# Optimization experiments

Hardware: AMD Instinct MI355X
Metric: run time of the kernel (lower is better)

## Reference

```python
import jax, jax.numpy as jnp
import numpy as np

NUM_EMBED = 1024
NUM_HEADS = 16
BLOCK_SIZE = 2048


def setup_inputs() -> dict:
    key = jax.random.key(0)
    k1, k2, k3, k4, k5 = jax.random.split(key, 5)
    C = NUM_EMBED
    s = 1.0 / np.sqrt(C)
    x = jax.random.normal(k1, (2, BLOCK_SIZE, C), dtype=jnp.float32)
    # nn.Linear params: weight (out,in), bias (out,)
    w_attn = jax.random.uniform(k2, (3 * C, C), minval=-s, maxval=s, dtype=jnp.float32)
    b_attn = jax.random.uniform(k3, (3 * C,), minval=-s, maxval=s, dtype=jnp.float32)
    w_proj = jax.random.uniform(k4, (C, C), minval=-s, maxval=s, dtype=jnp.float32)
    b_proj = jax.random.uniform(k5, (C,), minval=-s, maxval=s, dtype=jnp.float32)
    return {"x": x, "w_attn": w_attn, "b_attn": b_attn, "w_proj": w_proj, "b_proj": b_proj}


def reference(x, w_attn, b_attn, w_proj, b_proj):
    B, T, C = x.shape
    H = NUM_HEADS
    D = C // H
    kqv = jnp.einsum('btc,oc->bto', x, w_attn) + b_attn  # (B,T,3C)
    # Original code splits as K, Q, V in that order.
    K, Q, V = jnp.split(kqv, 3, axis=2)
    K = K.reshape(B, T, H, D).transpose(0, 2, 1, 3)  # (B,H,T,D)
    Q = Q.reshape(B, T, H, D).transpose(0, 2, 1, 3)
    V = V.reshape(B, T, H, D).transpose(0, 2, 1, 3)
    aff = jnp.einsum('bhqd,bhkd->bhqk', Q, K) * (D ** -0.5)  # (B,H,T,T)
    causal = jnp.tril(jnp.ones((T, T), dtype=bool))
    aff = jnp.where(causal[None, None], aff, jnp.float32(-jnp.inf))
    wei = jax.nn.softmax(aff, axis=-1)
    attn = jnp.einsum('bhqk,bhkd->bhqd', wei, V)
    attn = attn.transpose(0, 2, 1, 3).reshape(B, T, C)
    out = jnp.einsum('btc,oc->bto', attn, w_proj) + b_proj
    return out
```

## Files before the change

kernel.cpp:

```cpp
#include <hip/hip_runtime.h>
#include <cstdint>

typedef __attribute__((ext_vector_type(8))) short bf16x8;
typedef __attribute__((ext_vector_type(4))) float f32x4;
typedef __attribute__((ext_vector_type(4))) uint16_t u16x4;

__device__ __forceinline__ uint16_t f2b(float f) {
  union { float f; uint32_t i; } v; v.f = f;
  return (uint16_t)((v.i + 0x7FFFu + ((v.i >> 16) & 1u)) >> 16);
}

#define GLDS16(g, l) __builtin_amdgcn_global_load_lds( \
    (const __attribute__((address_space(1))) void*)(g), \
    (__attribute__((address_space(3))) void*)(l), 16, 0, 0)

__global__ __launch_bounds__(256) void cvt_f32_bf16(
    const float* __restrict__ src, uint16_t* __restrict__ dst, int n) {
  const int i = (blockIdx.x * 256 + threadIdx.x) * 4;
  if (i + 3 < n) {
    const float4 v = *(const float4*)(src + i);
    u16x4 o;
    o.x = f2b(v.x); o.y = f2b(v.y); o.z = f2b(v.z); o.w = f2b(v.w);
    *(u16x4*)(dst + i) = o;
  }
}

template <int BM, bool OUT_BF16>
__global__ __launch_bounds__(256) void gemm_bt_bias(
    const uint16_t* __restrict__ A, const uint16_t* __restrict__ B,
    const float* __restrict__ bias, void* __restrict__ Cv,
    int M, int N, int K) {
  constexpr int MI = BM / 32;
  constexpr int CA = BM / 16;
  constexpr int CPW = (2 * (CA + 8)) / 4;
  constexpr int CT_PITCH = OUT_BF16 ? 72 : 68;
  constexpr size_t CT_BYTES = (size_t)4 * (BM / 2) * CT_PITCH * (OUT_BF16 ? 2 : 4);
  constexpr size_t ST_BYTES = (size_t)(2 * (BM * 32 + 4096)) * 2;
  constexpr size_t LB = CT_BYTES > ST_BYTES ? CT_BYTES : ST_BYTES;
  __shared__ alignas(16) unsigned char ldsb[LB];
  uint16_t* lds = (uint16_t*)ldsb;
  const int offB0 = BM * 32;
  const int offA1 = BM * 32 + 4096;
  const int offB1 = 2 * BM * 32 + 4096;

  const int tid = threadIdx.x;
  const int wave = tid >> 6, lane = tid & 63;
  const int q4 = lane >> 4, l16 = lane & 15;
  const int wm = wave >> 1, wn = wave & 1;
  const long blockM = (long)blockIdx.y * BM;
  const long blockN = (long)blockIdx.x * 128;

  f32x4 acc[MI][4] = {};

  for (int k0 = 0; k0 < K; k0 += 64) {
#pragma unroll
    for (int c = 0; c < CPW; ++c) {
      const int id = c * 4 + wave;
      const uint16_t* mat; long rowBase; int a, kk, off;
      if (id < CA)               { mat = A; rowBase = blockM; a = id;            kk = k0;      off = 0; }
      else if (id < CA + 8)      { mat = B; rowBase = blockN; a = id - CA;       kk = k0;      off = offB0; }
      else if (id < 2 * CA + 8)  { mat = A; rowBase = blockM; a = id - CA - 8;   kk = k0 + 32; off = offA1; }
      else                       { mat = B; rowBase = blockN; a = id - 2*CA - 8; kk = k0 + 32; off = offB1; }
      const int flat = a * 64 + lane;
      const int row = flat >> 2, seg = flat & 3;
      GLDS16(mat + (rowBase + row) * (long)K + kk + seg * 8, lds + off + a * 512);
    }
    __syncthreads();
#pragma unroll
    for (int h = 0; h < 2; ++h) {
      const uint16_t* Ah = lds + (h ? offA1 : 0);
      const uint16_t* Bh = lds + (h ? offB1 : offB0);
      bf16x8 af[MI], bfr[4];
#pragma unroll
      for (int i = 0; i < MI; ++i)
        af[i] = *(const bf16x8*)&Ah[(wm * (BM / 2) + i * 16 + l16) * 32 + q4 * 8];
#pragma unroll
      for (int j = 0; j < 4; ++j)
        bfr[j] = *(const bf16x8*)&Bh[(wn * 64 + j * 16 + l16) * 32 + q4 * 8];
#pragma unroll
      for (int i = 0; i < MI; ++i)
#pragma unroll
        for (int j = 0; j < 4; ++j)
          acc[i][j] = __builtin_amdgcn_mfma_f32_16x16x32_bf16(af[i], bfr[j], acc[i][j], 0, 0, 0);
    }
    __syncthreads();
  }

  if (OUT_BF16) {
    uint16_t* ct = lds + wave * (BM / 2) * 72;
#pragma unroll
    for (int j = 0; j < 4; ++j) {
      const float bv = bias[blockN + wn * 64 + j * 16 + l16];
#pragma unroll
      for (int i = 0; i < MI; ++i)
#pragma unroll
        for (int r = 0; r < 4; ++r)
          ct[(i * 16 + q4 * 4 + r) * 72 + j * 16 + l16] = f2b(acc[i][j][r] + bv);
    }
    __syncthreads();
    uint16_t* Cb = (uint16_t*)Cv;
#pragma unroll
    for (int st = 0; st < BM / 16; ++st) {
      const int flat = st * 64 + lane;
      const int row = flat >> 3, seg = flat & 7;
      const bf16x8 v = *(const bf16x8*)&ct[row * 72 + seg * 8];
      *(bf16x8*)&Cb[(blockM + wm * (BM / 2) + row) * (long)N + blockN + wn * 64 + seg * 8] = v;
    }
  } else {
    float* ct = (float*)ldsb + wave * (BM / 2) * 68;
#pragma unroll
    for (int j = 0; j < 4; ++j) {
      const float bv = bias[blockN + wn * 64 + j * 16 + l16];
#pragma unroll
      for (int i = 0; i < MI; ++i)
#pragma unroll
        for (int r = 0; r < 4; ++r)
          ct[(i * 16 + q4 * 4 + r) * 68 + j * 16 + l16] = acc[i][j][r] + bv;
    }
    __syncthreads();
    float* Cb = (float*)Cv;
#pragma unroll
    for (int st = 0; st < BM / 8; ++st) {
      const int flat = st * 64 + lane;
      const int row = flat >> 4, seg = flat & 15;
      const f32x4 v = *(const f32x4*)&ct[row * 68 + seg * 4];
      *(f32x4*)&Cb[(blockM + wm * (BM / 2) + row) * (long)N + blockN + wn * 64 + seg * 4] = v;
    }
  }
}

__global__ __launch_bounds__(256, 4) void attn_flash(
    const uint16_t* __restrict__ kqv, uint16_t* __restrict__ attn) {
  constexpr int T = 2048, C = 1024, C3 = 3072, D = 64;
  __shared__ uint16_t KP[128 * 72];
  __shared__ uint16_t Vt[64 * 136];

  const int tid = threadIdx.x;
  const int wave = tid >> 6, lane = tid & 63;
  const int q4 = lane >> 4, l16 = lane & 15;
  const int bi = blockIdx.x;
  const int r4 = bi >> 8, jj = bi & 255;
  const int bh = jj & 31, u = jj >> 5;
  const int qb = r4 * 8 + ((r4 & 1) ? 7 - u : u);
  const int b = bh >> 4, h = bh & 15;

  const size_t base = (size_t)b * T * C3;
  uint16_t* Pt = &KP[wave * 2176];

  const int qrow_frag = qb * 64 + wave * 16 + l16;
  const bf16x8 qf0 = *(const bf16x8*)&kqv[base + (size_t)qrow_frag * C3 + C + h * D + q4 * 8];
  const bf16x8 qf1 = *(const bf16x8*)&kqv[base + (size_t)qrow_frag * C3 + C + h * D + 32 + q4 * 8];

  const int qrow = qb * 64 + wave * 16 + l16;
  f32x4 o[4] = {};
  float m_i = -1e30f, l_i = 0.f;

  const int nkt = (qb * 64 + 63) / 128 + 1;
  const float sc = 0.125f * 1.4426950408889634f;

  for (int kt = 0; kt < nkt; ++kt) {
    const int kbase = kt * 128;
    __syncthreads();
#pragma unroll
    for (int rr = 0; rr < 4; ++rr) {
      const int ci = rr * 256 + tid;
      const int row = ci >> 3, ch = ci & 7;
      *(bf16x8*)&KP[row * 72 + ch * 8] =
          *(const bf16x8*)&kqv[base + (size_t)(kbase + row) * C3 + h * D + ch * 8];
    }
    {
      uint32_t* VtW = (uint32_t*)Vt;
#pragma unroll
      for (int ss = 0; ss < 2; ++ss) {
        const int s = ss * 256 + tid;
        const int rp = s >> 3, ch = s & 7;
        const size_t g = base + (size_t)(kbase + 2 * rp) * C3 + 2 * C + h * D + ch * 8;
        const bf16x8 v0 = *(const bf16x8*)&kqv[g];
        const bf16x8 v1 = *(const bf16x8*)&kqv[g + C3];
        const int colw = (rp + 8 * ch) & 63;
#pragma unroll
        for (int i = 0; i < 8; ++i) {
          const uint32_t pack = (uint32_t)(uint16_t)((const short*)&v0)[i] |
                                ((uint32_t)(uint16_t)((const short*)&v1)[i] << 16);
          VtW[(ch * 8 + i) * 68 + colw] = pack;
        }
      }
    }
    __syncthreads();

    f32x4 s[8];
#pragma unroll
    for (int nk = 0; nk < 8; ++nk) {
      f32x4 z = {};
      const bf16x8 kf0 = *(const bf16x8*)&KP[(nk * 16 + l16) * 72 + q4 * 8];
      const bf16x8 kf1 = *(const bf16x8*)&KP[(nk * 16 + l16) * 72 + 32 + q4 * 8];
      z = __builtin_amdgcn_mfma_f32_16x16x32_bf16(kf0, qf0, z, 0, 0, 0);
      z = __builtin_amdgcn_mfma_f32_16x16x32_bf16(kf1, qf1, z, 0, 0, 0);
      s[nk] = z;
    }
    if (kbase + 127 > qb * 64 + wave * 16) {
#pragma unroll
      for (int nk = 0; nk < 8; ++nk) {
        const int key0 = kbase + nk * 16 + q4 * 4;
#pragma unroll
        for (int r = 0; r < 4; ++r)
          s[nk][r] = (key0 + r <= qrow) ? s[nk][r] : -1e30f;
      }
    }
    float mloc = s[0][0];
#pragma unroll
    for (int nk = 0; nk < 8; ++nk)
#pragma unroll
      for (int r = 0; r < 4; ++r) mloc = fmaxf(mloc, s[nk][r]);
    mloc = fmaxf(mloc, __shfl_xor(mloc, 16, 64));
    mloc = fmaxf(mloc, __shfl_xor(mloc, 32, 64));
    const float mnew = fmaxf(m_i, mloc * sc);
    const float alpha = exp2f(m_i - mnew);
    m_i = mnew;
    float rs = 0.f;
#pragma unroll
    for (int nk = 0; nk < 8; ++nk)
#pragma unroll
      for (int r = 0; r < 4; ++r) {
        const float p = exp2f(fmaf(s[nk][r], sc, -mnew));
        s[nk][r] = p;
        rs += p;
      }
    rs += __shfl_xor(rs, 16, 64);
    rs += __shfl_xor(rs, 32, 64);
    l_i = l_i * alpha + rs;
#pragma unroll
    for (int r = 0; r < 4; ++r) {
      const float ar = __shfl(alpha, q4 * 4 + r, 64);
#pragma unroll
      for (int d4 = 0; d4 < 4; ++d4) o[d4][r] *= ar;
    }
    __syncthreads();
#pragma unroll
    for (int nk = 0; nk < 8; ++nk) {
      uint32_t lo = (uint32_t)f2b(s[nk][0]) | ((uint32_t)f2b(s[nk][1]) << 16);
      uint32_t hi = (uint32_t)f2b(s[nk][2]) | ((uint32_t)f2b(s[nk][3]) << 16);
      uint2 pk; pk.x = lo; pk.y = hi;
      *(uint2*)&Pt[l16 * 136 + nk * 16 + q4 * 4] = pk;
    }
    __syncthreads();
#pragma unroll
    for (int ks = 0; ks < 4; ++ks) {
      const bf16x8 pf = *(const bf16x8*)&Pt[l16 * 136 + ks * 32 + q4 * 8];
#pragma unroll
      for (int d4 = 0; d4 < 4; ++d4) {
        const int d = d4 * 16 + l16;
        const int col = (ks * 32 + q4 * 8 + 16 * (d >> 3)) & 127;
        const bf16x8 vf = *(const bf16x8*)&Vt[d * 136 + col];
        o[d4] = __builtin_amdgcn_mfma_f32_16x16x32_bf16(pf, vf, o[d4], 0, 0, 0);
      }
    }
  }
  const size_t obase = (size_t)b * T * C;
  const float linv = 1.0f / l_i;
#pragma unroll
  for (int r = 0; r < 4; ++r) {
    const float lr = __shfl(linv, q4 * 4 + r, 64);
    const int q = qb * 64 + wave * 16 + q4 * 4 + r;
    const size_t rowoff = obase + (size_t)q * C + h * D;
#pragma unroll
    for (int d4 = 0; d4 < 4; ++d4)
      attn[rowoff + d4 * 16 + l16] = f2b(o[d4][r] * lr);
  }
}

extern "C" void kernel_launch(void* const* d_in, const int* in_sizes, int n_in,
                              void* d_out, int out_size, void* d_ws, size_t ws_size,
                              hipStream_t stream) {
  const float* x      = (const float*)d_in[0];
  const float* w_attn = (const float*)d_in[1];
  const float* b_attn = (const float*)d_in[2];
  const float* w_proj = (const float*)d_in[3];
  const float* b_proj = (const float*)d_in[4];
  float* out = (float*)d_out;

  uint16_t* xb    = (uint16_t*)d_ws;
  uint16_t* wab   = xb  + (size_t)4096 * 1024;
  uint16_t* wpb   = wab + (size_t)3072 * 1024;
  uint16_t* kqv   = wpb + (size_t)1024 * 1024;
  uint16_t* attnb = kqv + (size_t)4096 * 3072;

  dim3 blk(256, 1, 1);
  const int nx = 4096 * 1024, nwa = 3072 * 1024, nwp = 1024 * 1024;
  hipLaunchKernelGGL(cvt_f32_bf16, dim3(nx / 1024), blk, 0, stream, x, xb, nx);
  hipLaunchKernelGGL(cvt_f32_bf16, dim3(nwa / 1024), blk, 0, stream, w_attn, wab, nwa);
  hipLaunchKernelGGL(cvt_f32_bf16, dim3(nwp / 1024), blk, 0, stream, w_proj, wpb, nwp);

  hipLaunchKernelGGL((gemm_bt_bias<128, true>), dim3(3072 / 128, 4096 / 128, 1), blk, 0, stream,
                     xb, wab, b_attn, (void*)kqv, 4096, 3072, 1024);
  hipLaunchKernelGGL(attn_flash, dim3(1024, 1, 1), blk, 0, stream, kqv, attnb);
  hipLaunchKernelGGL((gemm_bt_bias<64, false>), dim3(1024 / 128, 4096 / 64, 1), blk, 0, stream,
                     attnb, wpb, b_proj, (void*)out, 4096, 1024, 1024);
}
```

Baseline: 201.6 us.

## Pair causal query blocks per workgroup, prefetch K/V to registers, fuse conversion kernels

```diff
diff --git a/kernel.cpp b/kernel.cpp
--- a/kernel.cpp
+++ b/kernel.cpp
@@ -1,4 +1,5 @@
 #include <hip/hip_runtime.h>
+#include <hip/hip_bf16.h>
 #include <cstdint>
 
 typedef __attribute__((ext_vector_type(8))) short bf16x8;
@@ -14,15 +15,18 @@
     (const __attribute__((address_space(1))) void*)(g), \
     (__attribute__((address_space(3))) void*)(l), 16, 0, 0)
 
-__global__ __launch_bounds__(256) void cvt_f32_bf16(
-    const float* __restrict__ src, uint16_t* __restrict__ dst, int n) {
+__global__ __launch_bounds__(256) void cvt_all(
+    const float* __restrict__ x, const float* __restrict__ wa, const float* __restrict__ wp,
+    uint16_t* __restrict__ xb, uint16_t* __restrict__ wab, uint16_t* __restrict__ wpb) {
   const int i = (blockIdx.x * 256 + threadIdx.x) * 4;
-  if (i + 3 < n) {
-    const float4 v = *(const float4*)(src + i);
-    u16x4 o;
-    o.x = f2b(v.x); o.y = f2b(v.y); o.z = f2b(v.z); o.w = f2b(v.w);
-    *(u16x4*)(dst + i) = o;
-  }
+  const float* src; uint16_t* dst; int off;
+  if (i < 4194304)      { src = x;  dst = xb;  off = i; }
+  else if (i < 7340032) { src = wa; dst = wab; off = i - 4194304; }
+  else                  { src = wp; dst = wpb; off = i - 7340032; }
+  const float4 v = *(const float4*)(src + off);
+  u16x4 o;
+  o.x = f2b(v.x); o.y = f2b(v.y); o.z = f2b(v.z); o.w = f2b(v.w);
+  *(u16x4*)(dst + off) = o;
 }
 
 template <int BM, bool OUT_BF16>
@@ -129,143 +133,162 @@
   }
 }
 
-__global__ __launch_bounds__(256, 4) void attn_flash(
+__global__ __launch_bounds__(256, 2) void attn_flash(
     const uint16_t* __restrict__ kqv, uint16_t* __restrict__ attn) {
-  constexpr int T = 2048, C = 1024, C3 = 3072, D = 64;
+  constexpr int T = 2048, C = 1024, C3 = 3072;
   __shared__ uint16_t KP[128 * 72];
   __shared__ uint16_t Vt[64 * 136];
+  uint32_t* VtW = (uint32_t*)Vt;
 
   const int tid = threadIdx.x;
   const int wave = tid >> 6, lane = tid & 63;
   const int q4 = lane >> 4, l16 = lane & 15;
-  const int bi = blockIdx.x;
-  const int r4 = bi >> 8, jj = bi & 255;
-  const int bh = jj & 31, u = jj >> 5;
-  const int qb = r4 * 8 + ((r4 & 1) ? 7 - u : u);
+  const int p = blockIdx.x >> 5, bh = blockIdx.x & 31;
   const int b = bh >> 4, h = bh & 15;
-
   const size_t base = (size_t)b * T * C3;
+  const int hD = h * 64;
+
   uint16_t* Pt = &KP[wave * 2176];
 
-  const int qrow_frag = qb * 64 + wave * 16 + l16;
-  const bf16x8 qf0 = *(const bf16x8*)&kqv[base + (size_t)qrow_frag * C3 + C + h * D + q4 * 8];
-  const bf16x8 qf1 = *(const bf16x8*)&kqv[base + (size_t)qrow_frag * C3 + C + h * D + 32 + q4 * 8];
-
-  const int qrow = qb * 64 + wave * 16 + l16;
-  f32x4 o[4] = {};
-  float m_i = -1e30f, l_i = 0.f;
-
-  const int nkt = (qb * 64 + 63) / 128 + 1;
+  const int tr = tid >> 3, kch = tid & 7;
   const float sc = 0.125f * 1.4426950408889634f;
 
-  for (int kt = 0; kt < nkt; ++kt) {
-    const int kbase = kt * 128;
-    __syncthreads();
-#pragma unroll
-    for (int rr = 0; rr < 4; ++rr) {
-      const int ci = rr * 256 + tid;
-      const int row = ci >> 3, ch = ci & 7;
-      *(bf16x8*)&KP[row * 72 + ch * 8] =
-          *(const bf16x8*)&kqv[base + (size_t)(kbase + row) * C3 + h * D + ch * 8];
-    }
-    {
-      uint32_t* VtW = (uint32_t*)Vt;
-#pragma unroll
-      for (int ss = 0; ss < 2; ++ss) {
-        const int s = ss * 256 + tid;
-        const int rp = s >> 3, ch = s & 7;
-        const size_t g = base + (size_t)(kbase + 2 * rp) * C3 + 2 * C + h * D + ch * 8;
-        const bf16x8 v0 = *(const bf16x8*)&kqv[g];
-        const bf16x8 v1 = *(const bf16x8*)&kqv[g + C3];
-        const int colw = (rp + 8 * ch) & 63;
+  for (int ss = 0; ss < 2; ++ss) {
+    const int qb = ss ? p : 31 - p;
+    const int nkt = (qb >> 1) + 1;
+    const int qrow = qb * 64 + wave * 16 + l16;
+    const bf16x8 qf0 = *(const bf16x8*)&kqv[base + (size_t)qrow * C3 + C + hD + q4 * 8];
+    const bf16x8 qf1 = *(const bf16x8*)&kqv[base + (size_t)qrow * C3 + C + hD + 32 + q4 * 8];
+
+    f32x4 o[4] = {};
+    float m_i = -1e30f, l_i = 0.f;
+
+    bf16x8 pk[4], pv0[2], pv1[2];
+#pragma unroll
+    for (int rr = 0; rr < 4; ++rr)
+      pk[rr] = *(const bf16x8*)&kqv[base + (size_t)(rr * 32 + tr) * C3 + hD + kch * 8];
+#pragma unroll
+    for (int s2 = 0; s2 < 2; ++s2) {
+      const size_t g = base + (size_t)(2 * (s2 * 32 + tr)) * C3 + 2 * C + hD + kch * 8;
+      pv0[s2] = *(const bf16x8*)&kqv[g];
+      pv1[s2] = *(const bf16x8*)&kqv[g + C3];
+    }
+
+    for (int kt = 0; kt < nkt; ++kt) {
+      const int kbase = kt * 128;
+      __syncthreads();
+#pragma unroll
+      for (int rr = 0; rr < 4; ++rr)
+        *(bf16x8*)&KP[(rr * 32 + tr) * 72 + kch * 8] = pk[rr];
+#pragma unroll
+      for (int s2 = 0; s2 < 2; ++s2) {
+        const int colw = ((s2 * 32 + tr) + 8 * kch) & 63;
+        const uint32_t* a0 = (const uint32_t*)&pv0[s2];
+        const uint32_t* a1 = (const uint32_t*)&pv1[s2];
 #pragma unroll
         for (int i = 0; i < 8; ++i) {
-          const uint32_t pack = (uint32_t)(uint16_t)((const short*)&v0)[i] |
-                                ((uint32_t)(uint16_t)((const short*)&v1)[i] << 16);
-          VtW[(ch * 8 + i) * 68 + colw] = pack;
-        }
-      }
-    }
-    __syncthreads();
-
-    f32x4 s[8];
-#pragma unroll
-    for (int nk = 0; nk < 8; ++nk) {
-      f32x4 z = {};
-      const bf16x8 kf0 = *(const bf16x8*)&KP[(nk * 16 + l16) * 72 + q4 * 8];
-      const bf16x8 kf1 = *(const bf16x8*)&KP[(nk * 16 + l16) * 72 + 32 + q4 * 8];
-      z = __builtin_amdgcn_mfma_f32_16x16x32_bf16(kf0, qf0, z, 0, 0, 0);
-      z = __builtin_amdgcn_mfma_f32_16x16x32_bf16(kf1, qf1, z, 0, 0, 0);
-      s[nk] = z;
-    }
-    if (kbase + 127 > qb * 64 + wave * 16) {
+          const uint32_t w = (i & 1)
+              ? __builtin_amdgcn_perm(a1[i >> 1], a0[i >> 1], 0x07060302u)
+              : __builtin_amdgcn_perm(a1[i >> 1], a0[i >> 1], 0x05040100u);
+          VtW[(kch * 8 + i) * 68 + colw] = w;
+        }
+      }
+      __syncthreads();
+      if (kt + 1 < nkt) {
+        const int kb = kbase + 128;
+#pragma unroll
+        for (int rr = 0; rr < 4; ++rr)
+          pk[rr] = *(const bf16x8*)&kqv[base + (size_t)(kb + rr * 32 + tr) * C3 + hD + kch * 8];
+#pragma unroll
+        for (int s2 = 0; s2 < 2; ++s2) {
+          const size_t g = base + (size_t)(kb + 2 * (s2 * 32 + tr)) * C3 + 2 * C + hD + kch * 8;
+          pv0[s2] = *(const bf16x8*)&kqv[g];
+          pv1[s2] = *(const bf16x8*)&kqv[g + C3];
+        }
+      }
+      f32x4 s[8];
 #pragma unroll
       for (int nk = 0; nk < 8; ++nk) {
-        const int key0 = kbase + nk * 16 + q4 * 4;
-#pragma unroll
-        for (int r = 0; r < 4; ++r)
-          s[nk][r] = (key0 + r <= qrow) ? s[nk][r] : -1e30f;
-      }
-    }
-    float mloc = s[0][0];
-#pragma unroll
-    for (int nk = 0; nk < 8; ++nk)
-#pragma unroll
-      for (int r = 0; r < 4; ++r) mloc = fmaxf(mloc, s[nk][r]);
-    mloc = fmaxf(mloc, __shfl_xor(mloc, 16, 64));
-    mloc = fmaxf(mloc, __shfl_xor(mloc, 32, 64));
-    const float mnew = fmaxf(m_i, mloc * sc);
-    const float alpha = exp2f(m_i - mnew);
-    m_i = mnew;
-    float rs = 0.f;
-#pragma unroll
-    for (int nk = 0; nk < 8; ++nk)
-#pragma unroll
-      for (int r = 0; r < 4; ++r) {
-        const float p = exp2f(fmaf(s[nk][r], sc, -mnew));
-        s[nk][r] = p;
-        rs += p;
-      }
-    rs += __shfl_xor(rs, 16, 64);
-    rs += __shfl_xor(rs, 32, 64);
-    l_i = l_i * alpha + rs;
+        f32x4 z = {};
+        const bf16x8 kf0 = *(const bf16x8*)&KP[(nk * 16 + l16) * 72 + q4 * 8];
+        const bf16x8 kf1 = *(const bf16x8*)&KP[(nk * 16 + l16) * 72 + 32 + q4 * 8];
+        z = __builtin_amdgcn_mfma_f32_16x16x32_bf16(kf0, qf0, z, 0, 0, 0);
+        z = __builtin_amdgcn_mfma_f32_16x16x32_bf16(kf1, qf1, z, 0, 0, 0);
+        s[nk] = z;
+      }
+      if (kbase + 127 > qb * 64 + wave * 16) {
+#pragma unroll
+        for (int nk = 0; nk < 8; ++nk) {
+          const int key0 = kbase + nk * 16 + q4 * 4;
+#pragma unroll
+          for (int r = 0; r < 4; ++r)
+            s[nk][r] = (key0 + r <= qrow) ? s[nk][r] : -1e30f;
+        }
+      }
+      float mloc = s[0][0];
+#pragma unroll
+      for (int nk = 0; nk < 8; ++nk)
+#pragma unroll
+        for (int r = 0; r < 4; ++r) mloc = fmaxf(mloc, s[nk][r]);
+      mloc = fmaxf(mloc, __shfl_xor(mloc, 16, 64));
+      mloc = fmaxf(mloc, __shfl_xor(mloc, 32, 64));
+      const float mnew = fmaxf(m_i, mloc * sc);
+      const float alpha = exp2f(m_i - mnew);
+      const bool mchg = mnew > m_i;
+      m_i = mnew;
+      float rs = 0.f;
+#pragma unroll
+      for (int nk = 0; nk < 8; ++nk)
+#pragma unroll
+        for (int r = 0; r < 4; ++r) {
+          const float pe = exp2f(fmaf(s[nk][r], sc, -mnew));
+          s[nk][r] = pe;
+          rs += pe;
+        }
+      rs += __shfl_xor(rs, 16, 64);
+      rs += __shfl_xor(rs, 32, 64);
+      l_i = l_i * alpha + rs;
+      if (__any(mchg)) {
+#pragma unroll
+        for (int r = 0; r < 4; ++r) {
+          const float ar = __shfl(alpha, q4 * 4 + r, 64);
+#pragma unroll
+          for (int d4 = 0; d4 < 4; ++d4) o[d4][r] *= ar;
+        }
+      }
+      __syncthreads();
+#pragma unroll
+      for (int nk = 0; nk < 8; ++nk) {
+        union { __hip_bfloat162 h2; uint32_t u; } c01, c23;
+        c01.h2 = __float22bfloat162_rn(make_float2(s[nk][0], s[nk][1]));
+        c23.h2 = __float22bfloat162_rn(make_float2(s[nk][2], s[nk][3]));
+        uint2 pkw; pkw.x = c01.u; pkw.y = c23.u;
+        *(uint2*)&Pt[l16 * 136 + nk * 16 + q4 * 4] = pkw;
+      }
+      __syncthreads();
+#pragma unroll
+      for (int ks = 0; ks < 4; ++ks) {
+        const bf16x8 pf = *(const bf16x8*)&Pt[l16 * 136 + ks * 32 + q4 * 8];
+#pragma unroll
+        for (int d4 = 0; d4 < 4; ++d4) {
+          const int d = d4 * 16 + l16;
+          const int col = (ks * 32 + q4 * 8 + 16 * (d >> 3)) & 127;
+          const bf16x8 vf = *(const bf16x8*)&Vt[d * 136 + col];
+          o[d4] = __builtin_amdgcn_mfma_f32_16x16x32_bf16(pf, vf, o[d4], 0, 0, 0);
+        }
+      }
+    }
+    const size_t obase = (size_t)b * T * C;
+    const float linv = 1.0f / l_i;
 #pragma unroll
     for (int r = 0; r < 4; ++r) {
-      const float ar = __shfl(alpha, q4 * 4 + r, 64);
-#pragma unroll
-      for (int d4 = 0; d4 < 4; ++d4) o[d4][r] *= ar;
-    }
-    __syncthreads();
-#pragma unroll
-    for (int nk = 0; nk < 8; ++nk) {
-      uint32_t lo = (uint32_t)f2b(s[nk][0]) | ((uint32_t)f2b(s[nk][1]) << 16);
-      uint32_t hi = (uint32_t)f2b(s[nk][2]) | ((uint32_t)f2b(s[nk][3]) << 16);
-      uint2 pk; pk.x = lo; pk.y = hi;
-      *(uint2*)&Pt[l16 * 136 + nk * 16 + q4 * 4] = pk;
-    }
-    __syncthreads();
-#pragma unroll
-    for (int ks = 0; ks < 4; ++ks) {
-      const bf16x8 pf = *(const bf16x8*)&Pt[l16 * 136 + ks * 32 + q4 * 8];
-#pragma unroll
-      for (int d4 = 0; d4 < 4; ++d4) {
-        const int d = d4 * 16 + l16;
-        const int col = (ks * 32 + q4 * 8 + 16 * (d >> 3)) & 127;
-        const bf16x8 vf = *(const bf16x8*)&Vt[d * 136 + col];
-        o[d4] = __builtin_amdgcn_mfma_f32_16x16x32_bf16(pf, vf, o[d4], 0, 0, 0);
-      }
-    }
-  }
-  const size_t obase = (size_t)b * T * C;
-  const float linv = 1.0f / l_i;
-#pragma unroll
-  for (int r = 0; r < 4; ++r) {
-    const float lr = __shfl(linv, q4 * 4 + r, 64);
-    const int q = qb * 64 + wave * 16 + q4 * 4 + r;
-    const size_t rowoff = obase + (size_t)q * C + h * D;
-#pragma unroll
-    for (int d4 = 0; d4 < 4; ++d4)
-      attn[rowoff + d4 * 16 + l16] = f2b(o[d4][r] * lr);
+      const float lr = __shfl(linv, q4 * 4 + r, 64);
+      const int q = qb * 64 + wave * 16 + q4 * 4 + r;
+      const size_t rowoff = obase + (size_t)q * C + hD;
+#pragma unroll
+      for (int d4 = 0; d4 < 4; ++d4)
+        attn[rowoff + d4 * 16 + l16] = f2b(o[d4][r] * lr);
+    }
   }
 }
 
@@ -286,14 +309,11 @@
   uint16_t* attnb = kqv + (size_t)4096 * 3072;
 
   dim3 blk(256, 1, 1);
-  const int nx = 4096 * 1024, nwa = 3072 * 1024, nwp = 1024 * 1024;
-  hipLaunchKernelGGL(cvt_f32_bf16, dim3(nx / 1024), blk, 0, stream, x, xb, nx);
-  hipLaunchKernelGGL(cvt_f32_bf16, dim3(nwa / 1024), blk, 0, stream, w_attn, wab, nwa);
-  hipLaunchKernelGGL(cvt_f32_bf16, dim3(nwp / 1024), blk, 0, stream, w_proj, wpb, nwp);
+  hipLaunchKernelGGL(cvt_all, dim3(8192), blk, 0, stream, x, w_attn, w_proj, xb, wab, wpb);
 
   hipLaunchKernelGGL((gemm_bt_bias<128, true>), dim3(3072 / 128, 4096 / 128, 1), blk, 0, stream,
                      xb, wab, b_attn, (void*)kqv, 4096, 3072, 1024);
-  hipLaunchKernelGGL(attn_flash, dim3(1024, 1, 1), blk, 0, stream, kqv, attnb);
+  hipLaunchKernelGGL(attn_flash, dim3(512, 1, 1), blk, 0, stream, kqv, attnb);
   hipLaunchKernelGGL((gemm_bt_bias<64, false>), dim3(1024 / 128, 4096 / 64, 1), blk, 0, stream,
                      attnb, wpb, b_proj, (void*)out, 4096, 1024, 1024);
 }
```

Result: faster. 193.6 us (-4.0%).
